# Kernel tuning notes

Hardware: AMD Instinct MI355X
Metric: run time of the kernel (lower is better)

## Reference

```python
import jax, jax.numpy as jnp
import numpy as np

N, E = 20000, 320000
IN, H, C = 1024, 8, 64
HC = H * C
EDGE_DIM = 16
NUM_GRAPHS = 8
LEAKY_SLOPE = 0.2
LN_EPS = 1e-5


def setup_inputs() -> dict:
    key = jax.random.key(0)
    ks = jax.random.split(key, 12)
    s = 0.05
    return {
        "x": jax.random.normal(ks[0], (N, IN), jnp.float32),
        "edge_attr": jax.random.normal(ks[1], (E, EDGE_DIM), jnp.float32),
        "edge_index": jax.random.randint(ks[2], (2, E), 0, N, dtype=jnp.int64),
        "batch": jnp.sort(jax.random.randint(ks[3], (N,), 0, NUM_GRAPHS, dtype=jnp.int64)),
        "W_src": jax.random.normal(ks[4], (IN, HC), jnp.float32) * s,
        "W_dst": jax.random.normal(ks[5], (IN, HC), jnp.float32) * s,
        "att_src": jax.random.normal(ks[6], (H, C), jnp.float32) * s,
        "att_dst": jax.random.normal(ks[7], (H, C), jnp.float32) * s,
        "bias": jnp.zeros((HC,), jnp.float32),
        "ln_gamma": jnp.ones((HC,), jnp.float32),
        "ln_beta": jnp.zeros((HC,), jnp.float32),
        "prelu_a": jnp.full((HC,), 0.25, jnp.float32),
    }


def reference(x, edge_attr, edge_index, batch, W_src, W_dst, att_src, att_dst,
              bias, ln_gamma, ln_beta, prelu_a):
    # Eval mode: node/edge feature dropout and attention dropout are identity.
    # with_edge == 'N': edge_attr is unused by the conv.
    n = x.shape[0]
    src, dst = edge_index[0], edge_index[1]

    xs = (x @ W_src).reshape(n, H, C)   # source-side projections
    xd = (x @ W_dst).reshape(n, H, C)   # dest-side projections
    a_src = jnp.einsum('nhc,hc->nh', xs, att_src)
    a_dst = jnp.einsum('nhc,hc->nh', xd, att_dst)

    # edge scores + softmax over incoming edges of each destination node
    e = jax.nn.leaky_relu(a_src[src] + a_dst[dst], LEAKY_SLOPE)  # [E,H]
    m = jax.ops.segment_max(e, dst, num_segments=n)              # [N,H]
    m = jax.lax.stop_gradient(jnp.where(jnp.isfinite(m), m, 0.0))
    ex = jnp.exp(e - m[dst])
    denom = jax.ops.segment_sum(ex, dst, num_segments=n)
    alpha = ex / (denom[dst] + 1e-16)                            # [E,H]

    msg = alpha[:, :, None] * xs[src]                            # [E,H,C]
    out = jax.ops.segment_sum(msg, dst, num_segments=n).reshape(n, HC) + bias

    # norm_type == 'layer': the per-graph boolean-mask loop applies LayerNorm
    # row-wise; with sorted batch ids this equals a single LayerNorm over all
    # nodes (LayerNorm has no cross-row statistics).
    mu = jnp.mean(out, axis=-1, keepdims=True)
    var = jnp.mean(jnp.square(out - mu), axis=-1, keepdims=True)
    y = (out - mu) * jax.lax.rsqrt(var + LN_EPS) * ln_gamma + ln_beta

    # PReLU with per-channel slope
    return jnp.where(y >= 0, y, prelu_a * y)
```

## Files before the change

kernel.cpp:

```cpp
#include <hip/hip_runtime.h>
#include <hip/hip_bf16.h>

#define N_NODES 20000
#define N_EDGES 320000
#define IN_DIM  1024
#define H_HEADS 8
#define C_CH    64
#define HC      512
#define LEAKY   0.2f
#define LN_EPS  1e-5f

#define BCOLS 576

typedef short bf16x8 __attribute__((ext_vector_type(8)));
typedef float f32x4  __attribute__((ext_vector_type(4)));

__device__ __forceinline__ unsigned short f2bf(float f) {
    union { float f; unsigned int u; } c; c.f = f;
    unsigned int u = c.u;
    unsigned int r = (u + 0x7fffu + ((u >> 16) & 1u)) >> 16;
    return (unsigned short)r;
}
__device__ __forceinline__ float bf2f(unsigned int h) {
    union { unsigned int u; float f; } c; c.u = h << 16; return c.f;
}
__device__ __forceinline__ void gload_lds16(const void* g, void* l) {
    __builtin_amdgcn_global_load_lds(
        (const __attribute__((address_space(1))) unsigned int*)g,
        (__attribute__((address_space(3))) unsigned int*)l, 16, 0, 0);
}

#define DEG_BLOCKS 1250
#define CONV_BLOCKS 2048

__global__ __launch_bounds__(256) void fused_pre(
        const float* __restrict__ x, short* __restrict__ xb,
        const int* __restrict__ ei, int* __restrict__ deg) {
    int t = threadIdx.x;
    if (blockIdx.x < DEG_BLOCKS) {
        int e = blockIdx.x * 256 + t;
        atomicAdd(&deg[ei[N_EDGES + e]], 1);
        return;
    }
    int bid = blockIdx.x - DEG_BLOCKS;
    const int total = N_NODES * IN_DIM / 8;
    int stride = CONV_BLOCKS * 256;
    for (int i = bid * 256 + t; i < total; i += stride) {
        float4 a = ((const float4*)x)[(size_t)i * 2];
        float4 b = ((const float4*)x)[(size_t)i * 2 + 1];
        uint4 r;
        r.x = (unsigned int)f2bf(a.x) | ((unsigned int)f2bf(a.y) << 16);
        r.y = (unsigned int)f2bf(a.z) | ((unsigned int)f2bf(a.w) << 16);
        r.z = (unsigned int)f2bf(b.x) | ((unsigned int)f2bf(b.y) << 16);
        r.w = (unsigned int)f2bf(b.z) | ((unsigned int)f2bf(b.w) << 16);
        *(uint4*)(&xb[(size_t)i * 8]) = r;
    }
}

__global__ void prep_w_scan(const float* __restrict__ Wsrc,
                            const float* __restrict__ Wdst,
                            const float* __restrict__ att_src,
                            const float* __restrict__ att_dst,
                            short* __restrict__ wbT,
                            const int* __restrict__ deg,
                            int* __restrict__ off,
                            int* __restrict__ cursor) {
    int t = threadIdx.x;

    if (blockIdx.x == IN_DIM) {
        __shared__ int wtot[2];
        int lane = t & 63, w = t >> 6;
        const int4* deg4 = (const int4*)deg;
        int s = 0;
        if (t < 125) {
            #pragma unroll
            for (int j = 0; j < 40; ++j) {
                int4 u = deg4[t * 40 + j];
                s += u.x + u.y + u.z + u.w;
            }
        }
        int v = s;
        #pragma unroll
        for (int o = 1; o < 64; o <<= 1) {
            int u = __shfl_up(v, o);
            if (lane >= o) v += u;
        }
        if (lane == 63) wtot[w] = v;
        __syncthreads();
        int add = (w == 1) ? wtot[0] : 0;
        int run = add + v - s;
        if (t < 125) {
            int4* off4 = (int4*)off;
            int4* cur4 = (int4*)cursor;
            #pragma unroll
            for (int j = 0; j < 40; ++j) {
                int4 u = deg4[t * 40 + j];
                int4 o_;
                o_.x = run;
                o_.y = o_.x + u.x;
                o_.z = o_.y + u.y;
                o_.w = o_.z + u.z;
                off4[t * 40 + j] = o_;
                cur4[t * 40 + j] = o_;
                run = o_.w + u.w;
            }
            if (t == 124) off[N_NODES] = run;
        }
        return;
    }

    int k = blockIdx.x;
    float4 v = *(const float4*)(Wsrc + (size_t)k * HC + t * 4);
    wbT[(size_t)(t * 4 + 0) * IN_DIM + k] = (short)f2bf(v.x);
    wbT[(size_t)(t * 4 + 1) * IN_DIM + k] = (short)f2bf(v.y);
    wbT[(size_t)(t * 4 + 2) * IN_DIM + k] = (short)f2bf(v.z);
    wbT[(size_t)(t * 4 + 3) * IN_DIM + k] = (short)f2bf(v.w);
    if (t < 16) {
        int h = t & 7;
        const float* W   = (t < 8) ? Wsrc : Wdst;
        const float* att = (t < 8) ? att_src : att_dst;
        float s = 0.f;
        #pragma unroll
        for (int c = 0; c < C_CH; ++c)
            s += W[(size_t)k * HC + h * C_CH + c] * att[h * C_CH + c];
        wbT[(size_t)(512 + t) * IN_DIM + k] = (short)f2bf(s);
    } else if (t < 64) {
        wbT[(size_t)(512 + t) * IN_DIM + k] = 0;
    }
}

#define BM 128
#define BN 96
#define BK 64
#define NCOLT (BCOLS / BN)
#define NROWT ((N_NODES + BM - 1) / BM)
#define NWG (NCOLT * NROWT)
#define KSTEPS (IN_DIM / BK)
#define A_SLOTS (BM * BK / 8)
#define B_SLOTS (BN * BK / 8)

__global__ __launch_bounds__(256) void gemm_scatter(
        const short* __restrict__ xb,
        const short* __restrict__ wbT,
        short* __restrict__ xsb,
        float* __restrict__ a_srcv,
        float* __restrict__ a_dstv,
        const int* __restrict__ ei,
        int* __restrict__ cursor,
        int* __restrict__ csr_src) {
    __shared__ short As[A_SLOTS * 8];
    __shared__ short Bs[B_SLOTS * 8];

    int t = threadIdx.x;

    if (blockIdx.x >= NWG) {
        int e = (blockIdx.x - NWG) * 256 + t;
        int d = ei[N_EDGES + e];
        int idx = atomicAdd(&cursor[d], 1);
        csr_src[idx] = ei[e];
        return;
    }

    int orig = blockIdx.x;
    const int q = NWG >> 3, r = NWG & 7;
    int xcd  = orig & 7;
    int wgid = (xcd < r ? xcd * (q + 1) : r * (q + 1) + (xcd - r) * q) + (orig >> 3);
    int col0 = (wgid % NCOLT) * BN;
    int row0 = (wgid / NCOLT) * BM;

    int lane = t & 63;
    int w    = t >> 6;
    int lr   = lane & 15;
    int lg   = lane >> 4;
    int sw   = lr & 7;
    int wr   = (w >> 1) * 64;
    int wc   = (w & 1) * 48;

    const short* a_base[4];
    #pragma unroll
    for (int i = 0; i < 4; ++i) {
        int s  = t + 256 * i;
        int m  = s >> 3;
        int kc = (s & 7) ^ (m & 7);
        int gm = row0 + m;
        if (gm >= N_NODES) gm = N_NODES - 1;
        a_base[i] = xb + (size_t)gm * IN_DIM + kc * 8;
    }
    const short* b_base[3];
    #pragma unroll
    for (int i = 0; i < 3; ++i) {
        int s  = t + 256 * i;
        int c  = s >> 3;
        int kc = (s & 7) ^ (c & 7);
        b_base[i] = wbT + (size_t)(col0 + c) * IN_DIM + kc * 8;
    }

    f32x4 acc[4][3] = {};

    for (int step = 0; step < KSTEPS; ++step) {
        int k0 = step * BK;
        #pragma unroll
        for (int i = 0; i < 4; ++i)
            gload_lds16(a_base[i] + k0, &As[(t + 256 * i) * 8]);
        #pragma unroll
        for (int i = 0; i < 3; ++i)
            gload_lds16(b_base[i] + k0, &Bs[(t + 256 * i) * 8]);
        asm volatile("s_waitcnt vmcnt(0)" ::: "memory");
        __builtin_amdgcn_s_barrier();

        #pragma unroll
        for (int ks = 0; ks < 2; ++ks) {
            int kc  = ks * 4 + lg;
            int kca = kc ^ sw;
            bf16x8 af[4], bfr[3];
            #pragma unroll
            for (int mi = 0; mi < 4; ++mi)
                af[mi] = *(const bf16x8*)(&As[((wr + mi * 16 + lr) * 8 + kca) * 8]);
            #pragma unroll
            for (int ni = 0; ni < 3; ++ni)
                bfr[ni] = *(const bf16x8*)(&Bs[((wc + ni * 16 + lr) * 8 + kca) * 8]);
            __builtin_amdgcn_s_setprio(1);
            #pragma unroll
            for (int mi = 0; mi < 4; ++mi)
                #pragma unroll
                for (int ni = 0; ni < 3; ++ni)
                    acc[mi][ni] = __builtin_amdgcn_mfma_f32_16x16x32_bf16(
                        af[mi], bfr[ni], acc[mi][ni], 0, 0, 0);
            __builtin_amdgcn_s_setprio(0);
        }
        __builtin_amdgcn_s_barrier();
    }

    #pragma unroll
    for (int mi = 0; mi < 4; ++mi) {
        #pragma unroll
        for (int rr = 0; rr < 4; ++rr) {
            int row = row0 + wr + mi * 16 + lg * 4 + rr;
            if (row >= N_NODES) continue;
            #pragma unroll
            for (int ni = 0; ni < 3; ++ni) {
                int col = col0 + wc + ni * 16 + lr;
                float v = acc[mi][ni][rr];
                if (col < 512)      xsb[(size_t)row * HC + col] = (short)f2bf(v);
                else if (col < 520) a_srcv[(size_t)row * 8 + (col - 512)] = v;
                else if (col < 528) a_dstv[(size_t)row * 8 + (col - 520)] = v;
            }
        }
    }
}

__global__ __launch_bounds__(256) void aggregate_ln(
        const int* __restrict__ off,
        const int* __restrict__ csr_src,
        const float* __restrict__ a_srcv,
        const float* __restrict__ a_dstv,
        const short* __restrict__ xsb,
        const float* __restrict__ bias,
        const float* __restrict__ gamma,
        const float* __restrict__ beta,
        const float* __restrict__ prelu_a,
        float* __restrict__ out) {
    int lane = threadIdx.x & 63;
    int n    = blockIdx.x * 4 + (threadIdx.x >> 6);
    int ch0  = lane * 8;
    int h    = lane >> 3;

    int start = off[n], end = off[n + 1];
    float ad  = a_dstv[(size_t)n * 8 + h];

    float acc[8] = {};
    float wsum = 0.f;

    int i = start;
    for (; i + 1 < end; i += 2) {
        int s0 = __builtin_amdgcn_readfirstlane(csr_src[i]);
        int s1 = __builtin_amdgcn_readfirstlane(csr_src[i + 1]);
        float sc0 = a_srcv[(size_t)s0 * 8 + h] + ad;
        float sc1 = a_srcv[(size_t)s1 * 8 + h] + ad;
        uint4 u0 = *(const uint4*)(xsb + (size_t)s0 * HC + ch0);
        uint4 u1 = *(const uint4*)(xsb + (size_t)s1 * HC + ch0);
        sc0 = (sc0 >= 0.f) ? sc0 : LEAKY * sc0;
        sc1 = (sc1 >= 0.f) ? sc1 : LEAKY * sc1;
        float w0 = __expf(sc0);
        float w1 = __expf(sc1);
        acc[0] = fmaf(w0, bf2f(u0.x & 0xffffu), acc[0]);
        acc[1] = fmaf(w0, bf2f(u0.x >> 16),     acc[1]);
        acc[2] = fmaf(w0, bf2f(u0.y & 0xffffu), acc[2]);
        acc[3] = fmaf(w0, bf2f(u0.y >> 16),     acc[3]);
        acc[4] = fmaf(w0, bf2f(u0.z & 0xffffu), acc[4]);
        acc[5] = fmaf(w0, bf2f(u0.z >> 16),     acc[5]);
        acc[6] = fmaf(w0, bf2f(u0.w & 0xffffu), acc[6]);
        acc[7] = fmaf(w0, bf2f(u0.w >> 16),     acc[7]);
        acc[0] = fmaf(w1, bf2f(u1.x & 0xffffu), acc[0]);
        acc[1] = fmaf(w1, bf2f(u1.x >> 16),     acc[1]);
        acc[2] = fmaf(w1, bf2f(u1.y & 0xffffu), acc[2]);
        acc[3] = fmaf(w1, bf2f(u1.y >> 16),     acc[3]);
        acc[4] = fmaf(w1, bf2f(u1.z & 0xffffu), acc[4]);
        acc[5] = fmaf(w1, bf2f(u1.z >> 16),     acc[5]);
        acc[6] = fmaf(w1, bf2f(u1.w & 0xffffu), acc[6]);
        acc[7] = fmaf(w1, bf2f(u1.w >> 16),     acc[7]);
        wsum += w0 + w1;
    }
    if (i < end) {
        int s0 = __builtin_amdgcn_readfirstlane(csr_src[i]);
        float sc0 = a_srcv[(size_t)s0 * 8 + h] + ad;
        uint4 u0 = *(const uint4*)(xsb + (size_t)s0 * HC + ch0);
        sc0 = (sc0 >= 0.f) ? sc0 : LEAKY * sc0;
        float w0 = __expf(sc0);
        acc[0] = fmaf(w0, bf2f(u0.x & 0xffffu), acc[0]);
        acc[1] = fmaf(w0, bf2f(u0.x >> 16),     acc[1]);
        acc[2] = fmaf(w0, bf2f(u0.y & 0xffffu), acc[2]);
        acc[3] = fmaf(w0, bf2f(u0.y >> 16),     acc[3]);
        acc[4] = fmaf(w0, bf2f(u0.z & 0xffffu), acc[4]);
        acc[5] = fmaf(w0, bf2f(u0.z >> 16),     acc[5]);
        acc[6] = fmaf(w0, bf2f(u0.w & 0xffffu), acc[6]);
        acc[7] = fmaf(w0, bf2f(u0.w >> 16),     acc[7]);
        wsum += w0;
    }

    float inv = 1.f / (wsum + 1e-16f);
    float4 b0 = *(const float4*)(bias + ch0);
    float4 b1 = *(const float4*)(bias + ch0 + 4);
    float v8[8];
    float psum = 0.f, psq = 0.f;
    const float bb[8] = {b0.x, b0.y, b0.z, b0.w, b1.x, b1.y, b1.z, b1.w};
    #pragma unroll
    for (int j = 0; j < 8; ++j) {
        v8[j] = acc[j] * inv + bb[j];
        psum += v8[j];
        psq  += v8[j] * v8[j];
    }
    #pragma unroll
    for (int o = 32; o > 0; o >>= 1) {
        psum += __shfl_xor(psum, o);
        psq  += __shfl_xor(psq, o);
    }
    float mu   = psum * (1.f / (float)HC);
    float var  = psq * (1.f / (float)HC) - mu * mu;
    float rstd = rsqrtf(var + LN_EPS);

    float4 g0 = *(const float4*)(gamma + ch0);
    float4 g1 = *(const float4*)(gamma + ch0 + 4);
    float4 e0 = *(const float4*)(beta + ch0);
    float4 e1 = *(const float4*)(beta + ch0 + 4);
    float4 p0 = *(const float4*)(prelu_a + ch0);
    float4 p1 = *(const float4*)(prelu_a + ch0 + 4);
    const float gg[8] = {g0.x, g0.y, g0.z, g0.w, g1.x, g1.y, g1.z, g1.w};
    const float ee[8] = {e0.x, e0.y, e0.z, e0.w, e1.x, e1.y, e1.z, e1.w};
    const float pp[8] = {p0.x, p0.y, p0.z, p0.w, p1.x, p1.y, p1.z, p1.w};
    float y[8];
    #pragma unroll
    for (int j = 0; j < 8; ++j) {
        float v = (v8[j] - mu) * rstd * gg[j] + ee[j];
        y[j] = (v >= 0.f) ? v : pp[j] * v;
    }
    float4* o4 = (float4*)(out + (size_t)n * HC + ch0);
    o4[0] = make_float4(y[0], y[1], y[2], y[3]);
    o4[1] = make_float4(y[4], y[5], y[6], y[7]);
}

extern "C" void kernel_launch(void* const* d_in, const int* in_sizes, int n_in,
                              void* d_out, int out_size, void* d_ws, size_t ws_size,
                              hipStream_t stream) {
    const float* x        = (const float*)d_in[0];
    const int*   ei       = (const int*)d_in[2];
    const float* Wsrc     = (const float*)d_in[4];
    const float* Wdst     = (const float*)d_in[5];
    const float* att_src  = (const float*)d_in[6];
    const float* att_dst  = (const float*)d_in[7];
    const float* bias     = (const float*)d_in[8];
    const float* gamma    = (const float*)d_in[9];
    const float* beta     = (const float*)d_in[10];
    const float* prelu_a  = (const float*)d_in[11];
    float* out            = (float*)d_out;

    char*  ws = (char*)d_ws;
    size_t o  = 0;
    auto alloc = [&](size_t bytes) -> void* {
        void* p = ws + o;
        o += (bytes + 255) & ~(size_t)255;
        return p;
    };
    short* wbT     = (short*)alloc(sizeof(short) * BCOLS * IN_DIM);
    short* xsb     = (short*)alloc(sizeof(short) * (size_t)N_NODES * HC);
    float* a_srcv  = (float*)alloc(sizeof(float) * N_NODES * 8);
    float* a_dstv  = (float*)alloc(sizeof(float) * N_NODES * 8);
    int*   deg     = (int*)alloc(sizeof(int) * N_NODES);
    int*   off     = (int*)alloc(sizeof(int) * (N_NODES + 1));
    int*   cursor  = (int*)alloc(sizeof(int) * N_NODES);
    int*   csr_src = (int*)alloc(sizeof(int) * N_EDGES);

    short* xb = (short*)d_out;

    hipMemsetAsync(deg, 0, sizeof(int) * N_NODES, stream);

    fused_pre<<<DEG_BLOCKS + CONV_BLOCKS, 256, 0, stream>>>(x, xb, ei, deg);

    prep_w_scan<<<IN_DIM + 1, 128, 0, stream>>>(Wsrc, Wdst, att_src, att_dst,
                                                wbT, deg, off, cursor);

    gemm_scatter<<<NWG + DEG_BLOCKS, 256, 0, stream>>>(
        xb, wbT, xsb, a_srcv, a_dstv, ei, cursor, csr_src);

    aggregate_ln<<<N_NODES / 4, 256, 0, stream>>>(
        off, csr_src, a_srcv, a_dstv, xsb, bias, gamma, beta, prelu_a, out);
}
```

Before: 165.8 us.

## Double-buffer GEMM LDS tiles with 128x128x32 tiling and async prefetch

Restructures the projection GEMM into a two-stage LDS pipeline that prefetches the next K-slice while computing the current one, waiting only on older loads. Tiles change from 128x96x64 to 128x128x32, which pads the weight matrix to 640 columns and changes the swizzle to 4 chunks. The goal is to hide global load latency behind MFMA work. The cost is extra padded columns of wasted compute (640 vs 576) and more barriers per K.

```diff
diff --git a/kernel.cpp b/kernel.cpp
--- a/kernel.cpp
+++ b/kernel.cpp
@@ -10,7 +10,7 @@
 #define LEAKY   0.2f
 #define LN_EPS  1e-5f
 
-#define BCOLS 576
+#define BCOLS 640
 
 typedef short bf16x8 __attribute__((ext_vector_type(8)));
 typedef float f32x4  __attribute__((ext_vector_type(4)));
@@ -124,14 +124,14 @@
         for (int c = 0; c < C_CH; ++c)
             s += W[(size_t)k * HC + h * C_CH + c] * att[h * C_CH + c];
         wbT[(size_t)(512 + t) * IN_DIM + k] = (short)f2bf(s);
-    } else if (t < 64) {
-        wbT[(size_t)(512 + t) * IN_DIM + k] = 0;
-    }
+    }
+    for (int j = 528 + t; j < BCOLS; j += 128)
+        wbT[(size_t)j * IN_DIM + k] = 0;
 }
 
 #define BM 128
-#define BN 96
-#define BK 64
+#define BN 128
+#define BK 32
 #define NCOLT (BCOLS / BN)
 #define NROWT ((N_NODES + BM - 1) / BM)
 #define NWG (NCOLT * NROWT)
@@ -148,8 +148,8 @@
         const int* __restrict__ ei,
         int* __restrict__ cursor,
         int* __restrict__ csr_src) {
-    __shared__ short As[A_SLOTS * 8];
-    __shared__ short Bs[B_SLOTS * 8];
+    __shared__ short As[2][A_SLOTS * 8];
+    __shared__ short Bs[2][B_SLOTS * 8];
 
     int t = threadIdx.x;
 
@@ -172,64 +172,73 @@
     int w    = t >> 6;
     int lr   = lane & 15;
     int lg   = lane >> 4;
-    int sw   = lr & 7;
     int wr   = (w >> 1) * 64;
-    int wc   = (w & 1) * 48;
-
-    const short* a_base[4];
-    #pragma unroll
-    for (int i = 0; i < 4; ++i) {
+    int wc   = (w & 1) * 64;
+    int kca  = lg ^ (lr & 3);
+
+    const short* a_base[2];
+    #pragma unroll
+    for (int i = 0; i < 2; ++i) {
         int s  = t + 256 * i;
-        int m  = s >> 3;
-        int kc = (s & 7) ^ (m & 7);
+        int m  = s >> 2;
+        int kc = (s & 3) ^ (m & 3);
         int gm = row0 + m;
         if (gm >= N_NODES) gm = N_NODES - 1;
         a_base[i] = xb + (size_t)gm * IN_DIM + kc * 8;
     }
-    const short* b_base[3];
-    #pragma unroll
-    for (int i = 0; i < 3; ++i) {
+    const short* b_base[2];
+    #pragma unroll
+    for (int i = 0; i < 2; ++i) {
         int s  = t + 256 * i;
-        int c  = s >> 3;
-        int kc = (s & 7) ^ (c & 7);
+        int c  = s >> 2;
+        int kc = (s & 3) ^ (c & 3);
         b_base[i] = wbT + (size_t)(col0 + c) * IN_DIM + kc * 8;
     }
 
-    f32x4 acc[4][3] = {};
-
+    f32x4 acc[4][4] = {};
+
+#define STAGE(buf, k0)                                                        \
+    do {                                                                      \
+        _Pragma("unroll")                                                     \
+        for (int i_ = 0; i_ < 2; ++i_)                                        \
+            gload_lds16(a_base[i_] + (k0), &As[buf][(t + 256 * i_) * 8]);     \
+        _Pragma("unroll")                                                     \
+        for (int i_ = 0; i_ < 2; ++i_)                                        \
+            gload_lds16(b_base[i_] + (k0), &Bs[buf][(t + 256 * i_) * 8]);     \
+    } while (0)
+
+    STAGE(0, 0);
+
+    int cur = 0;
     for (int step = 0; step < KSTEPS; ++step) {
-        int k0 = step * BK;
-        #pragma unroll
-        for (int i = 0; i < 4; ++i)
-            gload_lds16(a_base[i] + k0, &As[(t + 256 * i) * 8]);
-        #pragma unroll
-        for (int i = 0; i < 3; ++i)
-            gload_lds16(b_base[i] + k0, &Bs[(t + 256 * i) * 8]);
-        asm volatile("s_waitcnt vmcnt(0)" ::: "memory");
-        __builtin_amdgcn_s_barrier();
-
-        #pragma unroll
-        for (int ks = 0; ks < 2; ++ks) {
-            int kc  = ks * 4 + lg;
-            int kca = kc ^ sw;
-            bf16x8 af[4], bfr[3];
-            #pragma unroll
-            for (int mi = 0; mi < 4; ++mi)
-                af[mi] = *(const bf16x8*)(&As[((wr + mi * 16 + lr) * 8 + kca) * 8]);
-            #pragma unroll
-            for (int ni = 0; ni < 3; ++ni)
-                bfr[ni] = *(const bf16x8*)(&Bs[((wc + ni * 16 + lr) * 8 + kca) * 8]);
-            __builtin_amdgcn_s_setprio(1);
-            #pragma unroll
-            for (int mi = 0; mi < 4; ++mi)
-                #pragma unroll
-                for (int ni = 0; ni < 3; ++ni)
-                    acc[mi][ni] = __builtin_amdgcn_mfma_f32_16x16x32_bf16(
-                        af[mi], bfr[ni], acc[mi][ni], 0, 0, 0);
-            __builtin_amdgcn_s_setprio(0);
+        if (step + 1 < KSTEPS) {
+            STAGE(cur ^ 1, (step + 1) * BK);
+            asm volatile("s_waitcnt vmcnt(4)" ::: "memory");
+        } else {
+            asm volatile("s_waitcnt vmcnt(0)" ::: "memory");
         }
         __builtin_amdgcn_s_barrier();
-    }
+
+        bf16x8 af[4], bfr[4];
+        #pragma unroll
+        for (int mi = 0; mi < 4; ++mi)
+            af[mi] = *(const bf16x8*)(&As[cur][((wr + mi * 16 + lr) * 4 + kca) * 8]);
+        #pragma unroll
+        for (int ni = 0; ni < 4; ++ni)
+            bfr[ni] = *(const bf16x8*)(&Bs[cur][((wc + ni * 16 + lr) * 4 + kca) * 8]);
+        __builtin_amdgcn_s_setprio(1);
+        #pragma unroll
+        for (int mi = 0; mi < 4; ++mi)
+            #pragma unroll
+            for (int ni = 0; ni < 4; ++ni)
+                acc[mi][ni] = __builtin_amdgcn_mfma_f32_16x16x32_bf16(
+                    af[mi], bfr[ni], acc[mi][ni], 0, 0, 0);
+        __builtin_amdgcn_s_setprio(0);
+
+        __builtin_amdgcn_s_barrier();
+        cur ^= 1;
+    }
+#undef STAGE
 
     #pragma unroll
     for (int mi = 0; mi < 4; ++mi) {
@@ -238,7 +247,7 @@
             int row = row0 + wr + mi * 16 + lg * 4 + rr;
             if (row >= N_NODES) continue;
             #pragma unroll
-            for (int ni = 0; ni < 3; ++ni) {
+            for (int ni = 0; ni < 4; ++ni) {
                 int col = col0 + wc + ni * 16 + lr;
                 float v = acc[mi][ni][rr];
                 if (col < 512)      xsb[(size_t)row * HC + col] = (short)f2bf(v);
```

After: 193.4 us. 16.6% more time.
